# Optimization experiments

Hardware: AMD Instinct MI355X
Metric: run time of the kernel (lower is better)

The kernel has to match this reference:

```python
import jax, jax.numpy as jnp
import numpy as np

# Complex-YOLO / YOLOv2 anchors (anchor_step = 2)
ANCHORS = np.array([1.08, 1.19, 3.42, 4.41, 6.63, 11.38, 9.42, 5.11, 16.62, 10.52], np.float32).reshape(5, 2)
NA = 5          # num_anchors
NC = 8          # num_classes
COORD_SCALE = 1.0
NOOBJECT_SCALE = 1.0
OBJECT_SCALE = 10.0
CLASS_SCALE = 1.0
SIL_THRESH = 0.6

B, H, W, T = 32, 32, 64, 50


def setup_inputs() -> dict:
    key = jax.random.key(0)
    k1, k2 = jax.random.split(key)
    output = jax.random.normal(k1, (B, NA * (7 + NC), H, W), dtype=jnp.float32)
    # target layout: (cls, x, y, w, l, im, re), normalized coords in (0,1); col 1 != 0 => valid box
    target = jax.random.uniform(k2, (B, T, 7), dtype=jnp.float32, minval=0.01, maxval=1.0)
    return {"output": output, "target": target}


def _iou_cxcywh(b1, b2):
    # b1, b2: (..., 4) as (cx, cy, w, h); axis-aligned IoU, matching bbox_ious(x1y1x2y2=False)
    mx = jnp.minimum(b1[..., 0] - b1[..., 2] / 2, b2[..., 0] - b2[..., 2] / 2)
    Mx = jnp.maximum(b1[..., 0] + b1[..., 2] / 2, b2[..., 0] + b2[..., 2] / 2)
    my = jnp.minimum(b1[..., 1] - b1[..., 3] / 2, b2[..., 1] - b2[..., 3] / 2)
    My = jnp.maximum(b1[..., 1] + b1[..., 3] / 2, b2[..., 1] + b2[..., 3] / 2)
    cw = b1[..., 2] + b2[..., 2] - (Mx - mx)
    ch = b1[..., 3] + b2[..., 3] - (My - my)
    inter = jnp.where((cw > 0) & (ch > 0), cw * ch, 0.0)
    union = b1[..., 2] * b1[..., 3] + b2[..., 2] * b2[..., 3] - inter
    return inter / union


def _region_loss(output, target):
    nB, _, nH, nW = output.shape
    anc = jnp.asarray(ANCHORS)  # [NA, 2]
    out = output.reshape(nB, NA, 7 + NC, nH, nW)
    x = jax.nn.sigmoid(out[:, :, 0])
    y = jax.nn.sigmoid(out[:, :, 1])
    w = out[:, :, 2]
    l = out[:, :, 3]
    im = out[:, :, 4]
    re = out[:, :, 5]
    conf = jax.nn.sigmoid(out[:, :, 6])
    cls_logits = jnp.moveaxis(out[:, :, 7:], 2, -1)  # [B, A, H, W, C]

    # ---- decoded pred boxes (detached, like .data in torch) ----
    sg = jax.lax.stop_gradient
    grid_x = jnp.arange(nW, dtype=jnp.float32)
    grid_y = jnp.arange(nH, dtype=jnp.float32)
    pbx = sg(x) + grid_x[None, None, None, :]
    pby = sg(y) + grid_y[None, None, :, None]
    pbw = jnp.exp(sg(w)) * anc[None, :, 0, None, None]
    pbl = jnp.exp(sg(l)) * anc[None, :, 1, None, None]
    pred = jnp.stack([pbx, pby, pbw, pbl], axis=-1).reshape(nB, NA * nH * nW, 4)  # [B, N, 4]

    # ---- build_targets (fully vectorized) ----
    tgt = sg(target)
    nT = tgt.shape[1]
    valid = jnp.cumprod((tgt[..., 1] != 0).astype(jnp.int32), axis=1).astype(bool)  # break-on-zero semantics
    gx = tgt[..., 1] * nW
    gy = tgt[..., 2] * nH
    gw = tgt[..., 3] * nW
    gl = tgt[..., 4] * nH
    gi = jnp.clip(gx.astype(jnp.int32), 0, nW - 1)
    gj = jnp.clip(gy.astype(jnp.int32), 0, nH - 1)
    gt = jnp.stack([gx, gy, gw, gl], axis=-1)  # [B, T, 4]

    # IoU of every pred box against every GT -> silence mask
    ious = _iou_cxcywh(gt[:, :, None, :], pred[:, None, :, :])  # [B, T, N]
    ious = jnp.where(valid[..., None], ious, 0.0)
    max_iou = ious.max(axis=1)  # [B, N]
    conf_mask = jnp.where(max_iou > SIL_THRESH, 0.0, NOOBJECT_SCALE).reshape(nB, NA, nH, nW)

    # anchor matching: IoU of (0,0,gw,gl) vs (0,0,aw,ah) -> closed form
    inter_a = jnp.minimum(gw[..., None], anc[None, None, :, 0]) * jnp.minimum(gl[..., None], anc[None, None, :, 1])
    union_a = (gw * gl)[..., None] + (anc[:, 0] * anc[:, 1])[None, None, :] - inter_a
    a_iou = inter_a / union_a  # [B, T, A]
    best_n = jnp.argmax(a_iou, axis=-1)
    aw = anc[best_n, 0]
    al = anc[best_n, 1]

    # winner cell per GT; later GTs overwrite earlier ones at the same cell (torch loop order)
    b_idx = jnp.arange(nB)[:, None]
    lin = ((b_idx * NA + best_n) * nH + gj) * nW + gi  # [B, T]
    M = nB * NA * nH * nW
    t_eff = jnp.where(valid, jnp.arange(nT)[None, :], -1)
    seg = jax.ops.segment_max(t_eff.reshape(-1), lin.reshape(-1), num_segments=M)
    keep = valid & (t_eff == seg[lin])
    lin_safe = jnp.where(keep, lin, M).reshape(-1)  # route losers to dummy slot

    def scat(vals):
        return jnp.zeros(M + 1, jnp.float32).at[lin_safe].set(vals.reshape(-1))[:M].reshape(nB, NA, nH, nW)

    cm = scat(keep.astype(jnp.float32))           # coord_mask == cls_mask
    tx = scat(gx - gi)
    ty = scat(gy - gj)
    tw = scat(jnp.log(gw / aw))
    tl = scat(jnp.log(gl / al))
    tim = scat(tgt[..., 5])
    tre = scat(tgt[..., 6])
    tcls = scat(tgt[..., 0]).astype(jnp.int32)

    n_idx = best_n * (nH * nW) + gj * nW + gi
    pb = pred[b_idx, n_idx]                       # [B, T, 4] pred box at winner cell
    tconf = scat(_iou_cxcywh(gt, pb))
    conf_mask = jnp.where(cm > 0, OBJECT_SCALE, conf_mask)

    # ---- masked losses ----
    def mse(p, t):
        return jnp.sum((p * cm - t * cm) ** 2)

    loss_x = COORD_SCALE * mse(x, tx)
    loss_y = COORD_SCALE * mse(y, ty)
    loss_w = COORD_SCALE * mse(w, tw)
    loss_l = COORD_SCALE * mse(l, tl)
    loss_im = COORD_SCALE * mse(im, tim)
    loss_re = COORD_SCALE * mse(re, tre)
    loss_conf = jnp.sum((conf * conf_mask - tconf * conf_mask) ** 2)
    ce = jax.nn.logsumexp(cls_logits, axis=-1) - jnp.take_along_axis(cls_logits, tcls[..., None], axis=-1)[..., 0]
    loss_cls = CLASS_SCALE * jnp.sum(cm * ce)
    return loss_x + loss_y + loss_w + loss_l + loss_conf + loss_cls + loss_im + loss_re


def reference(output, target):
    return _region_loss(output, target)
```

## Files before the change

### kernel.cpp

```cpp
#include <hip/hip_runtime.h>
#include <math.h>

#define NB 32
#define NA 5
#define NC 8
#define NH 32
#define NW 64
#define NT 50
#define NCH (7 + NC)
#define HW (NH * NW)
#define OBJECT_SCALE 10.0f

__constant__ float c_anchors[NA * 2] = {
    1.08f, 1.19f, 3.42f, 4.41f, 6.63f, 11.38f, 9.42f, 5.11f, 16.62f, 10.52f};

__device__ __forceinline__ float sigmoidf(float v) {
    return 1.0f / (1.0f + expf(-v));
}

__global__ void prep_kernel(const float* __restrict__ target,
                            int* __restrict__ nvalid,
                            float* __restrict__ tinfo,
                            float* __restrict__ out) {
    int b = blockIdx.x;
    int t = threadIdx.x;
    const float* tp = target + (size_t)(b * NT + t) * 7;

    float t0 = 0.f, t1 = 0.f, t2 = 0.f, t3 = 0.f, t4 = 0.f, t5 = 0.f, t6 = 0.f;
    if (t < NT) {
        t0 = tp[0]; t1 = tp[1]; t2 = tp[2]; t3 = tp[3];
        t4 = tp[4]; t5 = tp[5]; t6 = tp[6];
    }
    unsigned long long bal = __ballot(t < NT && t1 != 0.0f);
    if (t == 0) {
        int nv = __ffsll((unsigned long long)~bal) - 1;
        nvalid[b] = nv;
        if (b == 0) out[0] = 0.0f;
    }
    if (t >= NT) return;

    float gx = t1 * (float)NW;
    float gy = t2 * (float)NH;
    float gw = t3 * (float)NW;
    float gl = t4 * (float)NH;

    int best_n = 0;
    float best = -1.0f;
#pragma unroll
    for (int a = 0; a < NA; ++a) {
        float aw = c_anchors[2 * a], al = c_anchors[2 * a + 1];
        float inter = fminf(gw, aw) * fminf(gl, al);
        float uni = gw * gl + aw * al - inter;
        float iou = inter / uni;
        if (iou > best) { best = iou; best_n = a; }
    }
    float aw = c_anchors[2 * best_n], al = c_anchors[2 * best_n + 1];

    int gi = min(max((int)gx, 0), NW - 1);
    int gj = min(max((int)gy, 0), NH - 1);

    float* ti = tinfo + (size_t)(b * NT + t) * 16;
    ti[0] = gx - gw * 0.5f;
    ti[1] = gx + gw * 0.5f;
    ti[2] = gy - gl * 0.5f;
    ti[3] = gy + gl * 0.5f;
    ti[4] = gw;
    ti[5] = gl;
    ti[6] = gw * gl;
    ti[7] = (float)((best_n << 12) | (gj << 6) | gi);
    ti[8] = gx - (float)gi;
    ti[9] = gy - (float)gj;
    ti[10] = t5;
    ti[11] = t6;
    ti[12] = t0;
    ti[13] = logf(gw / aw);
    ti[14] = logf(gl / al);
    ti[15] = 0.f;
}

__global__ __launch_bounds__(256) void cell_kernel(const float* __restrict__ output,
                                                   const float* __restrict__ tinfo,
                                                   const int* __restrict__ nvalid,
                                                   float* __restrict__ out) {
    const int blocks_per_b = (NA * HW) / 256;
    int b = blockIdx.x / blocks_per_b;
    int m = (blockIdx.x % blocks_per_b) * 256 + threadIdx.x;
    int a = m >> 11;
    int rem = m & (HW - 1);
    int j = rem >> 6;
    int i = rem & (NW - 1);

    const float* op = output + (size_t)(b * NA + a) * NCH * HW + (j << 6) + i;
    float o[NCH];
#pragma unroll
    for (int c = 0; c < NCH; ++c) o[c] = op[(size_t)c * HW];

    float x = sigmoidf(o[0]);
    float y = sigmoidf(o[1]);
    float conf = sigmoidf(o[6]);

    float aw = c_anchors[2 * a], al = c_anchors[2 * a + 1];
    float pbx = x + (float)i;
    float pby = y + (float)j;
    float pbw = expf(o[2]) * aw;
    float pbl = expf(o[3]) * al;

    float plx = pbx - pbw * 0.5f;
    float phx = pbx + pbw * 0.5f;
    float ply = pby - pbl * 0.5f;
    float phy = pby + pbl * 0.5f;
    float parea = pbw * pbl;
    float mycode = (float)((a << 12) | (j << 6) | i);

    int nv = nvalid[b];
    const float* tb = tinfo + (size_t)b * NT * 16;

    float silm = -1.0f;
    int ta = -1;
    for (int t = 0; t < nv; ++t) {
        const float* ti = tb + t * 16;
        float tlx = ti[0], thx = ti[1], tly = ti[2], thy = ti[3];
        float gw = ti[4], gl = ti[5], tarea = ti[6], code = ti[7];
        float mx = fminf(tlx, plx);
        float Mx = fmaxf(thx, phx);
        float my = fminf(tly, ply);
        float My = fmaxf(thy, phy);
        float cw = (gw + pbw) - (Mx - mx);
        float ch = (gl + pbl) - (My - my);
        float inter = (cw > 0.0f && ch > 0.0f) ? cw * ch : 0.0f;
        float uni = tarea + parea - inter;
        silm = fmaxf(silm, inter - 0.6f * uni);
        if (code == mycode) ta = t;
    }

    float loss;
    if (ta >= 0) {
        const float* ti = tb + (size_t)ta * 16;
        float tlx = ti[0], thx = ti[1], tly = ti[2], thy = ti[3];
        float gw = ti[4], gl = ti[5], tarea = ti[6];
        float mx = fminf(tlx, plx);
        float Mx = fmaxf(thx, phx);
        float my = fminf(tly, ply);
        float My = fmaxf(thy, phy);
        float cw = (gw + pbw) - (Mx - mx);
        float ch = (gl + pbl) - (My - my);
        float inter = (cw > 0.0f && ch > 0.0f) ? cw * ch : 0.0f;
        float tconf = inter / (tarea + parea - inter);

        float dx = x - ti[8];
        float dy = y - ti[9];
        float dw = o[2] - ti[13];
        float dl = o[3] - ti[14];
        float di = o[4] - ti[10];
        float dr = o[5] - ti[11];
        loss = dx * dx + dy * dy + dw * dw + dl * dl + di * di + dr * dr;

        float dc = OBJECT_SCALE * (conf - tconf);
        loss += dc * dc;

        int tcls = min(max((int)ti[12], 0), NC - 1);
        float mxl = o[7];
#pragma unroll
        for (int c = 1; c < NC; ++c) mxl = fmaxf(mxl, o[7 + c]);
        float s = 0.0f;
#pragma unroll
        for (int c = 0; c < NC; ++c) s += expf(o[7 + c] - mxl);
        loss += (mxl + logf(s)) - o[7 + tcls];
    } else {
        loss = (silm > 0.0f) ? 0.0f : conf * conf;
    }

    for (int off = 32; off > 0; off >>= 1)
        loss += __shfl_down(loss, off, 64);
    __shared__ float s_part[4];
    int wave = threadIdx.x >> 6;
    int lane = threadIdx.x & 63;
    if (lane == 0) s_part[wave] = loss;
    __syncthreads();
    if (threadIdx.x == 0)
        atomicAdd(out, s_part[0] + s_part[1] + s_part[2] + s_part[3]);
}

extern "C" void kernel_launch(void* const* d_in, const int* in_sizes, int n_in,
                              void* d_out, int out_size, void* d_ws, size_t ws_size,
                              hipStream_t stream) {
    const float* output = (const float*)d_in[0];
    const float* target = (const float*)d_in[1];
    float* out = (float*)d_out;
    int* nvalid = (int*)d_ws;
    float* tinfo = (float*)((char*)d_ws + 128);

    hipLaunchKernelGGL(prep_kernel, dim3(NB), dim3(64), 0, stream,
                       target, nvalid, tinfo, out);
    hipLaunchKernelGGL(cell_kernel, dim3(NB * 40), dim3(256), 0, stream,
                       output, tinfo, nvalid, out);
}
```

Measured before the change: 95.08 us.

## Load class logits only for target-owning cells and use fast math intrinsics

Defers the eight class-logit channel loads to the branch taken only by cells assigned a ground-truth box, cutting global memory reads for nearly all cells. Replaces exp/log/sigmoid with fast hardware intrinsics. Precomputes the scaled target area and rewrites the ignore-threshold test so the per-target loop needs fewer operations. Fast intrinsics slightly reduce numerical accuracy.

```diff
diff --git a/kernel.cpp b/kernel.cpp
--- a/kernel.cpp
+++ b/kernel.cpp
@@ -14,8 +14,10 @@
 __constant__ float c_anchors[NA * 2] = {
     1.08f, 1.19f, 3.42f, 4.41f, 6.63f, 11.38f, 9.42f, 5.11f, 16.62f, 10.52f};
 
-__device__ __forceinline__ float sigmoidf(float v) {
-    return 1.0f / (1.0f + expf(-v));
+__device__ __forceinline__ float fast_exp(float v) { return __expf(v); }
+__device__ __forceinline__ float fast_log(float v) { return __logf(v); }
+__device__ __forceinline__ float fast_sigmoid(float v) {
+    return __builtin_amdgcn_rcpf(1.0f + __expf(-v));
 }
 
 __global__ void prep_kernel(const float* __restrict__ target,
@@ -60,22 +62,23 @@
     int gj = min(max((int)gy, 0), NH - 1);
 
     float* ti = tinfo + (size_t)(b * NT + t) * 16;
+    float area = gw * gl;
     ti[0] = gx - gw * 0.5f;
     ti[1] = gx + gw * 0.5f;
     ti[2] = gy - gl * 0.5f;
     ti[3] = gy + gl * 0.5f;
     ti[4] = gw;
     ti[5] = gl;
-    ti[6] = gw * gl;
+    ti[6] = 0.6f * area;
     ti[7] = (float)((best_n << 12) | (gj << 6) | gi);
     ti[8] = gx - (float)gi;
     ti[9] = gy - (float)gj;
     ti[10] = t5;
     ti[11] = t6;
     ti[12] = t0;
-    ti[13] = logf(gw / aw);
-    ti[14] = logf(gl / al);
-    ti[15] = 0.f;
+    ti[13] = fast_log(gw / aw);
+    ti[14] = fast_log(gl / al);
+    ti[15] = area;
 }
 
 __global__ __launch_bounds__(256) void cell_kernel(const float* __restrict__ output,
@@ -91,19 +94,18 @@
     int i = rem & (NW - 1);
 
     const float* op = output + (size_t)(b * NA + a) * NCH * HW + (j << 6) + i;
-    float o[NCH];
-#pragma unroll
-    for (int c = 0; c < NCH; ++c) o[c] = op[(size_t)c * HW];
-
-    float x = sigmoidf(o[0]);
-    float y = sigmoidf(o[1]);
-    float conf = sigmoidf(o[6]);
+    float o0 = op[0 * HW], o1 = op[1 * HW], o2 = op[2 * HW], o3 = op[3 * HW];
+    float o4 = op[4 * HW], o5 = op[5 * HW], o6 = op[6 * HW];
+
+    float x = fast_sigmoid(o0);
+    float y = fast_sigmoid(o1);
+    float conf = fast_sigmoid(o6);
 
     float aw = c_anchors[2 * a], al = c_anchors[2 * a + 1];
     float pbx = x + (float)i;
     float pby = y + (float)j;
-    float pbw = expf(o[2]) * aw;
-    float pbl = expf(o[3]) * al;
+    float pbw = fast_exp(o2) * aw;
+    float pbl = fast_exp(o3) * al;
 
     float plx = pbx - pbw * 0.5f;
     float phx = pbx + pbw * 0.5f;
@@ -115,21 +117,20 @@
     int nv = nvalid[b];
     const float* tb = tinfo + (size_t)b * NT * 16;
 
-    float silm = -1.0f;
+    float silm = -1e30f;
     int ta = -1;
     for (int t = 0; t < nv; ++t) {
         const float* ti = tb + t * 16;
         float tlx = ti[0], thx = ti[1], tly = ti[2], thy = ti[3];
-        float gw = ti[4], gl = ti[5], tarea = ti[6], code = ti[7];
+        float gw = ti[4], gl = ti[5], ct = ti[6], code = ti[7];
         float mx = fminf(tlx, plx);
         float Mx = fmaxf(thx, phx);
         float my = fminf(tly, ply);
         float My = fmaxf(thy, phy);
-        float cw = (gw + pbw) - (Mx - mx);
-        float ch = (gl + pbl) - (My - my);
-        float inter = (cw > 0.0f && ch > 0.0f) ? cw * ch : 0.0f;
-        float uni = tarea + parea - inter;
-        silm = fmaxf(silm, inter - 0.6f * uni);
+        float cw = gw + pbw - (Mx - mx);
+        float ch = gl + pbl - (My - my);
+        float inter = fmaxf(cw, 0.0f) * fmaxf(ch, 0.0f);
+        silm = fmaxf(silm, 1.6f * inter - ct);
         if (code == mycode) ta = t;
     }
 
@@ -137,37 +138,41 @@
     if (ta >= 0) {
         const float* ti = tb + (size_t)ta * 16;
         float tlx = ti[0], thx = ti[1], tly = ti[2], thy = ti[3];
-        float gw = ti[4], gl = ti[5], tarea = ti[6];
+        float gw = ti[4], gl = ti[5], tarea = ti[15];
         float mx = fminf(tlx, plx);
         float Mx = fmaxf(thx, phx);
         float my = fminf(tly, ply);
         float My = fmaxf(thy, phy);
-        float cw = (gw + pbw) - (Mx - mx);
-        float ch = (gl + pbl) - (My - my);
-        float inter = (cw > 0.0f && ch > 0.0f) ? cw * ch : 0.0f;
+        float cw = gw + pbw - (Mx - mx);
+        float ch = gl + pbl - (My - my);
+        float inter = fmaxf(cw, 0.0f) * fmaxf(ch, 0.0f);
         float tconf = inter / (tarea + parea - inter);
 
         float dx = x - ti[8];
         float dy = y - ti[9];
-        float dw = o[2] - ti[13];
-        float dl = o[3] - ti[14];
-        float di = o[4] - ti[10];
-        float dr = o[5] - ti[11];
+        float dw = o2 - ti[13];
+        float dl = o3 - ti[14];
+        float di = o4 - ti[10];
+        float dr = o5 - ti[11];
         loss = dx * dx + dy * dy + dw * dw + dl * dl + di * di + dr * dr;
 
         float dc = OBJECT_SCALE * (conf - tconf);
         loss += dc * dc;
 
+        float cl[NC];
+#pragma unroll
+        for (int c = 0; c < NC; ++c) cl[c] = op[(size_t)(7 + c) * HW];
         int tcls = min(max((int)ti[12], 0), NC - 1);
-        float mxl = o[7];
-#pragma unroll
-        for (int c = 1; c < NC; ++c) mxl = fmaxf(mxl, o[7 + c]);
+        float mxl = cl[0];
+#pragma unroll
+        for (int c = 1; c < NC; ++c) mxl = fmaxf(mxl, cl[c]);
         float s = 0.0f;
 #pragma unroll
-        for (int c = 0; c < NC; ++c) s += expf(o[7 + c] - mxl);
-        loss += (mxl + logf(s)) - o[7 + tcls];
+        for (int c = 0; c < NC; ++c) s += fast_exp(cl[c] - mxl);
+        loss += (mxl + fast_log(s)) - cl[tcls];
     } else {
-        loss = (silm > 0.0f) ? 0.0f : conf * conf;
+        bool silenced = silm > 0.6f * parea;
+        loss = silenced ? 0.0f : conf * conf;
     }
 
     for (int off = 32; off > 0; off >>= 1)
```

Measured after the change: 92.07 us. 1.03x faster.
